# Performance work log

Measured on AMD Instinct MI355X. Metric: run time of the kernel, lower is better.

The kernel has to match this reference:

```python
import jax, jax.numpy as jnp
import numpy as np

NUM_GRAPHS = 1024
NODES_PER_GRAPH = 256
NUM_NODES = NUM_GRAPHS * NODES_PER_GRAPH  # 262144
EMBED_DIM = 300
EPS = 1e-12


def setup_inputs() -> dict:
    key = jax.random.key(0)
    tensor = jax.random.normal(key, (NUM_NODES, EMBED_DIM), dtype=jnp.float32)
    # per-graph node counts; equal-sized graphs summing exactly to NUM_NODES
    batch_list = jnp.full((NUM_GRAPHS,), NODES_PER_GRAPH, dtype=jnp.int64)
    return {"tensor": tensor, "batch_list": batch_list}


def reference(tensor, batch_list):
    # tensor: [N, D] node features; batch_list: [B] nodes per graph
    B = batch_list.shape[0]
    N = tensor.shape[0]
    # segment id per node (repeat_interleave of graph index)
    seg = jnp.repeat(jnp.arange(B), batch_list, total_repeat_length=N)  # [N]
    tmax = jax.ops.segment_max(tensor, seg, num_segments=B)  # [B, D]
    tmin = jax.ops.segment_min(tensor, seg, num_segments=B)  # [B, D]
    mid = (tmax + tmin) * 0.5
    ldv = (tmax - tmin) * 0.5
    # gather per-graph stats back to nodes (repeat)
    mid_n = mid[seg]                       # [N, D]
    ldv_n = jnp.maximum(ldv[seg], EPS)     # clamp: ldv[ldv<=1e-12]=1e-12
    return (tensor - mid_n) / ldv_n
```

## Files before the change

kernel.cpp:

```cpp
#include <hip/hip_runtime.h>
#include <float.h>


#define NUM_GRAPHS 1024
#define NODES      256
#define DIMS       300
#define CHUNK      64
#define NCHUNK     5
#define EPS        1e-12f

__device__ __forceinline__ float4 f4min(float4 a, float4 b) {
    return make_float4(fminf(a.x, b.x), fminf(a.y, b.y),
                       fminf(a.z, b.z), fminf(a.w, b.w));
}
__device__ __forceinline__ float4 f4max(float4 a, float4 b) {
    return make_float4(fmaxf(a.x, b.x), fmaxf(a.y, b.y),
                       fmaxf(a.z, b.z), fmaxf(a.w, b.w));
}

__global__ __launch_bounds__(256) void cube_norm_kernel(
    const float* __restrict__ in, float* __restrict__ out)
{
    const int chunk = blockIdx.x;
    const int g     = blockIdx.y;
    const int tid   = threadIdx.x;
    const int x     = tid & 15;
    const int y     = tid >> 4;
    const int d0    = chunk * CHUNK + x * 4;
    const bool active = d0 < DIMS;

    const size_t graph_base = (size_t)g * NODES * DIMS;

    float4 vals[16];
    float4 vmin = make_float4( FLT_MAX,  FLT_MAX,  FLT_MAX,  FLT_MAX);
    float4 vmax = make_float4(-FLT_MAX, -FLT_MAX, -FLT_MAX, -FLT_MAX);

    if (active) {
#pragma unroll
        for (int i = 0; i < 16; ++i) {
            const int node = i * 16 + y;
            const float4 v = *(const float4*)(in + graph_base + (size_t)node * DIMS + d0);
            vals[i] = v;
            vmin = f4min(vmin, v);
            vmax = f4max(vmax, v);
        }
    }

    __shared__ float4 smin[16][16];
    __shared__ float4 smax[16][16];
    __shared__ float4 smid[16];
    __shared__ float4 sinv[16];

    smin[y][x] = vmin;
    smax[y][x] = vmax;
    __syncthreads();

    if (tid < 16) {
        float4 mn = smin[0][tid];
        float4 mx = smax[0][tid];
#pragma unroll
        for (int j = 1; j < 16; ++j) {
            mn = f4min(mn, smin[j][tid]);
            mx = f4max(mx, smax[j][tid]);
        }
        float4 mid, inv;
        mid.x = (mx.x + mn.x) * 0.5f;
        mid.y = (mx.y + mn.y) * 0.5f;
        mid.z = (mx.z + mn.z) * 0.5f;
        mid.w = (mx.w + mn.w) * 0.5f;
        inv.x = 1.0f / fmaxf((mx.x - mn.x) * 0.5f, EPS);
        inv.y = 1.0f / fmaxf((mx.y - mn.y) * 0.5f, EPS);
        inv.z = 1.0f / fmaxf((mx.z - mn.z) * 0.5f, EPS);
        inv.w = 1.0f / fmaxf((mx.w - mn.w) * 0.5f, EPS);
        smid[tid] = mid;
        sinv[tid] = inv;
    }
    __syncthreads();

    if (active) {
        const float4 mid = smid[x];
        const float4 inv = sinv[x];
#pragma unroll
        for (int i = 0; i < 16; ++i) {
            const int node = i * 16 + y;
            const float4 v = vals[i];
            float4 o;
            o.x = (v.x - mid.x) * inv.x;
            o.y = (v.y - mid.y) * inv.y;
            o.z = (v.z - mid.z) * inv.z;
            o.w = (v.w - mid.w) * inv.w;
            *(float4*)(out + graph_base + (size_t)node * DIMS + d0) = o;
        }
    }
}

extern "C" void kernel_launch(void* const* d_in, const int* in_sizes, int n_in,
                              void* d_out, int out_size, void* d_ws, size_t ws_size,
                              hipStream_t stream) {
    const float* tensor = (const float*)d_in[0];
    float* out = (float*)d_out;

    dim3 grid(NCHUNK, NUM_GRAPHS);
    dim3 block(256);
    cube_norm_kernel<<<grid, block, 0, stream>>>(tensor, out);
}
```

Before: 557.8 us.

## Use wave shuffles for min/max reduction, drop a barrier, nontemporal stores

Replaces the shared-memory 16x16 min/max reduction with xor shuffles within each wave, followed by a small 4-entry cross-wave combine that every thread performs itself. This removes the second __syncthreads and the serial 16-thread reduction step. Output writes become nontemporal stores so the write-once data does not pollute the cache. It also raises the launch-bounds occupancy hint and adds asm barriers on the loads to keep them issued early. The main cost is memory bandwidth, so the expected gain is limited, and the occupancy hint could cause register spills.

```diff
diff --git a/kernel.cpp b/kernel.cpp
--- a/kernel.cpp
+++ b/kernel.cpp
@@ -9,6 +9,8 @@
 #define NCHUNK     5
 #define EPS        1e-12f
 
+typedef float v4f __attribute__((ext_vector_type(4)));
+
 __device__ __forceinline__ float4 f4min(float4 a, float4 b) {
     return make_float4(fminf(a.x, b.x), fminf(a.y, b.y),
                        fminf(a.z, b.z), fminf(a.w, b.w));
@@ -18,7 +20,7 @@
                        fmaxf(a.z, b.z), fmaxf(a.w, b.w));
 }
 
-__global__ __launch_bounds__(256) void cube_norm_kernel(
+__global__ __launch_bounds__(256, 4) void cube_norm_kernel(
     const float* __restrict__ in, float* __restrict__ out)
 {
     const int chunk = blockIdx.x;
@@ -26,10 +28,14 @@
     const int tid   = threadIdx.x;
     const int x     = tid & 15;
     const int y     = tid >> 4;
+    const int wv    = tid >> 6;
+    const int lane  = tid & 63;
     const int d0    = chunk * CHUNK + x * 4;
     const bool active = d0 < DIMS;
 
     const size_t graph_base = (size_t)g * NODES * DIMS;
+    const float* gin  = in  + graph_base;
+    float*       gout = out + graph_base;
 
     float4 vals[16];
     float4 vmin = make_float4( FLT_MAX,  FLT_MAX,  FLT_MAX,  FLT_MAX);
@@ -39,57 +45,57 @@
 #pragma unroll
         for (int i = 0; i < 16; ++i) {
             const int node = i * 16 + y;
-            const float4 v = *(const float4*)(in + graph_base + (size_t)node * DIMS + d0);
+            float4 v = *(const float4*)(gin + (size_t)node * DIMS + d0);
+            asm volatile("" : "+v"(v.x), "+v"(v.y), "+v"(v.z), "+v"(v.w));
             vals[i] = v;
             vmin = f4min(vmin, v);
             vmax = f4max(vmax, v);
         }
     }
 
-    __shared__ float4 smin[16][16];
-    __shared__ float4 smax[16][16];
-    __shared__ float4 smid[16];
-    __shared__ float4 sinv[16];
+#pragma unroll
+    for (int s = 16; s <= 32; s += s) {
+        vmin.x = fminf(vmin.x, __shfl_xor(vmin.x, s));
+        vmin.y = fminf(vmin.y, __shfl_xor(vmin.y, s));
+        vmin.z = fminf(vmin.z, __shfl_xor(vmin.z, s));
+        vmin.w = fminf(vmin.w, __shfl_xor(vmin.w, s));
+        vmax.x = fmaxf(vmax.x, __shfl_xor(vmax.x, s));
+        vmax.y = fmaxf(vmax.y, __shfl_xor(vmax.y, s));
+        vmax.z = fmaxf(vmax.z, __shfl_xor(vmax.z, s));
+        vmax.w = fmaxf(vmax.w, __shfl_xor(vmax.w, s));
+    }
 
-    smin[y][x] = vmin;
-    smax[y][x] = vmax;
+    __shared__ float4 smn[4][16];
+    __shared__ float4 smx[4][16];
+    if (lane < 16) { smn[wv][lane] = vmin; smx[wv][lane] = vmax; }
     __syncthreads();
 
-    if (tid < 16) {
-        float4 mn = smin[0][tid];
-        float4 mx = smax[0][tid];
-#pragma unroll
-        for (int j = 1; j < 16; ++j) {
-            mn = f4min(mn, smin[j][tid]);
-            mx = f4max(mx, smax[j][tid]);
-        }
-        float4 mid, inv;
-        mid.x = (mx.x + mn.x) * 0.5f;
-        mid.y = (mx.y + mn.y) * 0.5f;
-        mid.z = (mx.z + mn.z) * 0.5f;
-        mid.w = (mx.w + mn.w) * 0.5f;
-        inv.x = 1.0f / fmaxf((mx.x - mn.x) * 0.5f, EPS);
-        inv.y = 1.0f / fmaxf((mx.y - mn.y) * 0.5f, EPS);
-        inv.z = 1.0f / fmaxf((mx.z - mn.z) * 0.5f, EPS);
-        inv.w = 1.0f / fmaxf((mx.w - mn.w) * 0.5f, EPS);
-        smid[tid] = mid;
-        sinv[tid] = inv;
-    }
-    __syncthreads();
+    const float4 mn = f4min(f4min(smn[0][x], smn[1][x]),
+                            f4min(smn[2][x], smn[3][x]));
+    const float4 mx = f4max(f4max(smx[0][x], smx[1][x]),
+                            f4max(smx[2][x], smx[3][x]));
+
+    float4 mid, inv;
+    mid.x = (mx.x + mn.x) * 0.5f;
+    mid.y = (mx.y + mn.y) * 0.5f;
+    mid.z = (mx.z + mn.z) * 0.5f;
+    mid.w = (mx.w + mn.w) * 0.5f;
+    inv.x = 1.0f / fmaxf((mx.x - mn.x) * 0.5f, EPS);
+    inv.y = 1.0f / fmaxf((mx.y - mn.y) * 0.5f, EPS);
+    inv.z = 1.0f / fmaxf((mx.z - mn.z) * 0.5f, EPS);
+    inv.w = 1.0f / fmaxf((mx.w - mn.w) * 0.5f, EPS);
 
     if (active) {
-        const float4 mid = smid[x];
-        const float4 inv = sinv[x];
 #pragma unroll
         for (int i = 0; i < 16; ++i) {
             const int node = i * 16 + y;
             const float4 v = vals[i];
-            float4 o;
-            o.x = (v.x - mid.x) * inv.x;
-            o.y = (v.y - mid.y) * inv.y;
-            o.z = (v.z - mid.z) * inv.z;
-            o.w = (v.w - mid.w) * inv.w;
-            *(float4*)(out + graph_base + (size_t)node * DIMS + d0) = o;
+            v4f o = { (v.x - mid.x) * inv.x,
+                      (v.y - mid.y) * inv.y,
+                      (v.z - mid.z) * inv.z,
+                      (v.w - mid.w) * inv.w };
+            __builtin_nontemporal_store(
+                o, (v4f*)(gout + (size_t)node * DIMS + d0));
         }
     }
 }
```

After: 603.6 us. +8.2%, slower.
